# Optimization experiments

Hardware: AMD Instinct MI355X
Metric: run time of the kernel (lower is better)

The kernel has to match this reference:

```python
import jax, jax.numpy as jnp
import numpy as np

DIM = 768
HEADS = 12
HEAD_DIM = DIM // HEADS
EPS = 1e-5

def setup_inputs() -> dict:
    key = jax.random.key(0)
    ks = jax.random.split(key, 12)
    s = 1.0 / np.sqrt(DIM)
    x = jax.random.normal(ks[0], (4, 2048, DIM), dtype=jnp.float32)
    Wq = jax.random.uniform(ks[1], (DIM, DIM), jnp.float32, -s, s)
    bq = jnp.zeros((DIM,), jnp.float32)
    Wk = jax.random.uniform(ks[2], (DIM, DIM), jnp.float32, -s, s)
    bk = jnp.zeros((DIM,), jnp.float32)
    Wv = jax.random.uniform(ks[3], (DIM, DIM), jnp.float32, -s, s)
    bv = jnp.zeros((DIM,), jnp.float32)
    W1 = jax.random.uniform(ks[4], (DIM, 2 * DIM), jnp.float32, -s, s)
    b1 = jnp.zeros((2 * DIM,), jnp.float32)
    s2 = 1.0 / np.sqrt(2 * DIM)
    W2 = jax.random.uniform(ks[5], (2 * DIM, DIM), jnp.float32, -s2, s2)
    b2 = jnp.zeros((DIM,), jnp.float32)
    gamma = jnp.ones((DIM,), jnp.float32)
    beta = jnp.zeros((DIM,), jnp.float32)
    return {"x": x, "Wq": Wq, "bq": bq, "Wk": Wk, "bk": bk, "Wv": Wv, "bv": bv,
            "W1": W1, "b1": b1, "W2": W2, "b2": b2, "gamma": gamma, "beta": beta}

def reference(x, Wq, bq, Wk, bk, Wv, bv, W1, b1, W2, b2, gamma, beta):
    B, S, _ = x.shape
    # QKV projections -> (B, H, S, Dh)
    q = (x @ Wq + bq).reshape(B, S, HEADS, HEAD_DIM).transpose(0, 2, 1, 3)
    k = (x @ Wk + bk).reshape(B, S, HEADS, HEAD_DIM).transpose(0, 2, 1, 3)
    v = (x @ Wv + bv).reshape(B, S, HEADS, HEAD_DIM).transpose(0, 2, 1, 3)
    scores = jnp.einsum('bhqd,bhkd->bhqk', q, k) / jnp.sqrt(jnp.float32(HEAD_DIM))
    attn = jax.nn.softmax(scores, axis=-1)  # dropout is identity in eval
    ctx = jnp.einsum('bhqk,bhkd->bhqd', attn, v)
    ctx = ctx.transpose(0, 2, 1, 3).reshape(B, S, DIM)
    # MLP
    out = jax.nn.relu(ctx @ W1 + b1) @ W2 + b2
    # residual + LayerNorm
    h = x + out
    mu = jnp.mean(h, axis=-1, keepdims=True)
    var = jnp.mean(jnp.square(h - mu), axis=-1, keepdims=True)
    return (h - mu) * jax.lax.rsqrt(var + EPS) * gamma + beta
```

## Files before the change

### kernel.cpp

```cpp
#include <hip/hip_runtime.h>
#include <stdint.h>

#define DIM 768
#define HDIM 64
#define NHEADS 12
#define SEQ 2048
#define BATCH 4
#define NTOK (BATCH*SEQ)
#define FF 1536
#define QSCALE 0.1803368801111204f

typedef __bf16 bf16x8 __attribute__((ext_vector_type(8)));
typedef float f32x4 __attribute__((ext_vector_type(4)));
typedef unsigned short u16;
typedef unsigned int u32;

static __device__ __forceinline__ u16 f2bf(float f) {
  u32 u = __float_as_uint(f);
  u32 r = (u + 0x7fffu + ((u >> 16) & 1u)) >> 16;
  return (u16)r;
}

static __device__ __forceinline__ void async16(const void* g, void* l) {
  __builtin_amdgcn_global_load_lds(
      (const __attribute__((address_space(1))) u32*)g,
      (__attribute__((address_space(3))) u32*)l, 16, 0, 0);
}


__global__ void conv_bf16(const float* __restrict__ in, u16* __restrict__ out, int n) {
  int i = (blockIdx.x * 256 + threadIdx.x) * 4;
  if (i < n) {
    float4 f = *(const float4*)(in + i);
    uint2 o;
    o.x = (u32)f2bf(f.x) | ((u32)f2bf(f.y) << 16);
    o.y = (u32)f2bf(f.z) | ((u32)f2bf(f.w) << 16);
    *(uint2*)(out + i) = o;
  }
}

__global__ void prep_weights(const float* __restrict__ Wq, const float* __restrict__ Wk,
                             const float* __restrict__ Wv, const float* __restrict__ W1,
                             const float* __restrict__ W2, const float* __restrict__ bq,
                             const float* __restrict__ bk, const float* __restrict__ bv,
                             u16* __restrict__ Wqkvt, u16* __restrict__ W1t,
                             u16* __restrict__ W2t, float* __restrict__ bqkv) {
  const int bid = blockIdx.x;
  if (bid >= 4032) {
    int i = (bid - 4032) * 256 + threadIdx.x;
    if (i < DIM) bqkv[i] = bq[i];
    else if (i < 2 * DIM) bqkv[i] = bk[i - DIM];
    else if (i < 3 * DIM) bqkv[i] = bv[i - 2 * DIM];
    return;
  }
  const float* W; u16* dst; int K, N, tile;
  if (bid < 1728) {
    int z = bid / 576, t2 = bid - z * 576;
    W = z == 0 ? Wq : (z == 1 ? Wk : Wv);
    dst = Wqkvt + (size_t)z * DIM * DIM; K = DIM; N = DIM; tile = t2;
  } else if (bid < 2880) {
    W = W1; dst = W1t; K = DIM; N = FF; tile = bid - 1728;
  } else {
    W = W2; dst = W2t; K = FF; N = DIM; tile = bid - 2880;
  }
  const int ntx = N / 32;
  const int k0 = (tile / ntx) * 32, n0 = (tile - (tile / ntx) * ntx) * 32;
  __shared__ float t32[32][33];
  const int tx = threadIdx.x & 31, ty = threadIdx.x >> 5;
#pragma unroll
  for (int i = 0; i < 4; i++)
    t32[ty + 8 * i][tx] = W[(size_t)(k0 + ty + 8 * i) * N + n0 + tx];
  __syncthreads();
#pragma unroll
  for (int i = 0; i < 4; i++)
    dst[(size_t)(n0 + ty + 8 * i) * K + k0 + tx] = f2bf(t32[tx][ty + 8 * i]);
}


template<int MODE, int NT>
__launch_bounds__(256, 3)
__global__ void gemm128(const u16* __restrict__ A, const u16* __restrict__ Bt,
                        const float* __restrict__ bias, void* __restrict__ outp,
                        int K) {
  __shared__ u16 sA[128 * 64];
  __shared__ u16 sB[128 * 64];
  const int t = threadIdx.x;
  const int w = t >> 6;
  const int lane = t & 63;
  const int quad = lane >> 4;
  const int l15 = lane & 15;

  const int fid = blockIdx.x;
  const int xcd = fid & 7;
  const int j = fid >> 3;
  const int m0 = (xcd + 8 * (j / NT)) * 128;
  const int n0 = (j % NT) * 128;

  const int wr = (w & 1) * 64;
  const int wc = (w >> 1) * 64;

  f32x4 acc[4][4];
#pragma unroll
  for (int i = 0; i < 4; i++)
#pragma unroll
    for (int jj = 0; jj < 4; jj++) acc[i][jj] = (f32x4){0.f, 0.f, 0.f, 0.f};

  const int rowA = lane >> 3;
  const int colSw = ((lane & 7) ^ rowA) * 8;

  for (int k0 = 0; k0 < K; k0 += 64) {
    __syncthreads();
#pragma unroll
    for (int jj = 0; jj < 4; jj++) {
      int r0 = (jj * 4 + w) * 8;
      async16(A + (size_t)(m0 + r0 + rowA) * K + k0 + colSw, sA + r0 * 64);
      async16(Bt + (size_t)(n0 + r0 + rowA) * K + k0 + colSw, sB + r0 * 64);
    }
    __builtin_amdgcn_s_waitcnt(0);
    __syncthreads();
#pragma unroll
    for (int ks = 0; ks < 64; ks += 32) {
      bf16x8 a[4], b[4];
#pragma unroll
      for (int i = 0; i < 4; i++)
        a[i] = *(const bf16x8*)(sA + (wr + i * 16 + l15) * 64 +
                                ((((ks >> 3) + quad) ^ (l15 & 7)) * 8));
#pragma unroll
      for (int jj = 0; jj < 4; jj++)
        b[jj] = *(const bf16x8*)(sB + (wc + jj * 16 + l15) * 64 +
                                 ((((ks >> 3) + quad) ^ (l15 & 7)) * 8));
#pragma unroll
      for (int i = 0; i < 4; i++)
#pragma unroll
        for (int jj = 0; jj < 4; jj++)
          acc[i][jj] = __builtin_amdgcn_mfma_f32_16x16x32_bf16(a[i], b[jj], acc[i][jj], 0, 0, 0);
    }
  }

#pragma unroll
  for (int i = 0; i < 4; i++) {
#pragma unroll
    for (int jj = 0; jj < 4; jj++) {
#pragma unroll
      for (int r = 0; r < 4; r++) {
        int m = m0 + wr + i * 16 + quad * 4 + r;
        int n = n0 + wc + jj * 16 + l15;
        float v = acc[i][jj][r] + bias[n];
        if (MODE == 5) {
          int b = m >> 11, s = m & 2047;
          u16* o = (u16*)outp;
          if (n < DIM) {
            int h = n >> 6, d = n & 63;
            o[(((size_t)(b * NHEADS + h) * SEQ + s) << 6) + d] = f2bf(v * QSCALE);
          } else if (n < 2 * DIM) {
            int nn = n - DIM, h = nn >> 6, d = nn & 63;
            o[(size_t)NTOK * DIM + (((size_t)(b * NHEADS + h) * SEQ + s) << 6) + d] = f2bf(v);
          } else {
            int nn = n - 2 * DIM, h = nn >> 6, d = nn & 63;
            o[2 * (size_t)NTOK * DIM + ((size_t)(b * NHEADS + h) * HDIM + d) * SEQ + s] = f2bf(v);
          }
        } else if (MODE == 3) {
          ((u16*)outp)[(size_t)m * FF + n] = f2bf(fmaxf(v, 0.f));
        } else {
          ((float*)outp)[(size_t)m * DIM + n] = v;
        }
      }
    }
  }
}


__launch_bounds__(256, 3)
__global__ void attn(const u16* __restrict__ Q, const u16* __restrict__ Kb,
                     const u16* __restrict__ Vt, u16* __restrict__ Ctx) {
  __shared__ u16 sK[2][64 * 64];
  __shared__ u16 sV[2][64 * 64];
  __shared__ u16 sP[4][32 * 64];
  const int t = threadIdx.x, w = t >> 6, lane = t & 63;
  const int quad = lane >> 4, l15 = lane & 15;

  const int fid = blockIdx.x;
  const int xcd = fid & 7;
  const int idx = fid >> 3;
  const int bh = xcd + 8 * (idx >> 4);
  const int qb = idx & 15;
  const size_t qkbase = (size_t)bh * SEQ * HDIM;
  const int q0 = qb * 128 + w * 32;

  bf16x8 qf[2][2];
#pragma unroll
  for (int i = 0; i < 2; i++)
#pragma unroll
    for (int ks = 0; ks < 2; ks++)
      qf[i][ks] = *(const bf16x8*)(Q + qkbase + (size_t)(q0 + i * 16 + l15) * HDIM +
                                   ks * 32 + quad * 8);

  f32x4 o[2][4];
#pragma unroll
  for (int i = 0; i < 2; i++)
#pragma unroll
    for (int di = 0; di < 4; di++) o[i][di] = (f32x4){0.f, 0.f, 0.f, 0.f};
  float rs[2] = {0.f, 0.f};

  const int rowK = lane >> 3;
  const int colKsw = ((lane & 7) ^ rowK) * 8;
  const int swz = l15 & 7;

#define STAGE(kt, b) do {                                                          \
    int rr0 = w * 8, rr1 = (4 + w) * 8;                                            \
    async16(Kb + qkbase + (size_t)((kt) * 64 + rr0 + rowK) * HDIM + colKsw,        \
            sK[b] + rr0 * 64);                                                     \
    async16(Vt + qkbase + (size_t)(rr0 + rowK) * SEQ + (kt) * 64 + colKsw,         \
            sV[b] + rr0 * 64);                                                     \
    async16(Kb + qkbase + (size_t)((kt) * 64 + rr1 + rowK) * HDIM + colKsw,        \
            sK[b] + rr1 * 64);                                                     \
    async16(Vt + qkbase + (size_t)(rr1 + rowK) * SEQ + (kt) * 64 + colKsw,         \
            sV[b] + rr1 * 64);                                                     \
  } while (0)

  auto compute = [&](int cur) {
    const u16* kb = sK[cur];
    const u16* vb = sV[cur];
    u16* pw = sP[w];

    f32x4 sc[2][4];
    __builtin_amdgcn_s_setprio(1);
#pragma unroll
    for (int n4 = 0; n4 < 4; n4++) {
      int kr = n4 * 16;
      bf16x8 a0 = *(const bf16x8*)(kb + (kr + l15) * 64 + ((quad ^ swz) * 8));
      bf16x8 a1 = *(const bf16x8*)(kb + (kr + l15) * 64 + (((4 + quad) ^ swz) * 8));
#pragma unroll
      for (int i = 0; i < 2; i++) {
        f32x4 c = (f32x4){0.f, 0.f, 0.f, 0.f};
        c = __builtin_amdgcn_mfma_f32_16x16x32_bf16(a0, qf[i][0], c, 0, 0, 0);
        c = __builtin_amdgcn_mfma_f32_16x16x32_bf16(a1, qf[i][1], c, 0, 0, 0);
        sc[i][n4] = c;
      }
    }
    __builtin_amdgcn_s_setprio(0);

#pragma unroll
    for (int i = 0; i < 2; i++) {
      int row = i * 16 + l15;
#pragma unroll
      for (int n4 = 0; n4 < 4; n4++) {
        float p0 = __builtin_amdgcn_exp2f(sc[i][n4][0]);
        float p1 = __builtin_amdgcn_exp2f(sc[i][n4][1]);
        float p2 = __builtin_amdgcn_exp2f(sc[i][n4][2]);
        float p3 = __builtin_amdgcn_exp2f(sc[i][n4][3]);
        rs[i] += (p0 + p1) + (p2 + p3);
        u32 lo, hi;
        asm("v_cvt_pk_bf16_f32 %0, %1, %2" : "=v"(lo) : "v"(p0), "v"(p1));
        asm("v_cvt_pk_bf16_f32 %0, %1, %2" : "=v"(hi) : "v"(p2), "v"(p3));
        int cp = (n4 * 2 + (quad >> 1)) ^ swz;
        *(uint2*)(pw + row * 64 + cp * 8 + (quad & 1) * 4) = (uint2){lo, hi};
      }
    }

    __builtin_amdgcn_s_setprio(1);
#pragma unroll
    for (int ks = 0; ks < 2; ks++) {
      bf16x8 ap[2];
#pragma unroll
      for (int i = 0; i < 2; i++)
        ap[i] = *(const bf16x8*)(pw + (i * 16 + l15) * 64 + (((ks * 4 + quad) ^ swz) * 8));
#pragma unroll
      for (int di = 0; di < 4; di++) {
        bf16x8 b = *(const bf16x8*)(vb + (di * 16 + l15) * 64 +
                                    (((ks * 4 + quad) ^ swz) * 8));
        o[0][di] = __builtin_amdgcn_mfma_f32_16x16x32_bf16(ap[0], b, o[0][di], 0, 0, 0);
        o[1][di] = __builtin_amdgcn_mfma_f32_16x16x32_bf16(ap[1], b, o[1][di], 0, 0, 0);
      }
    }
    __builtin_amdgcn_s_setprio(0);
  };

  STAGE(0, 0);
  int cur = 0;
  for (int kt = 0; kt < SEQ / 64 - 1; kt++) {
    STAGE(kt + 1, cur ^ 1);
    asm volatile("s_waitcnt vmcnt(4)" ::: "memory");
    __builtin_amdgcn_s_barrier();
    compute(cur);
    __builtin_amdgcn_s_barrier();
    cur ^= 1;
  }
  asm volatile("s_waitcnt vmcnt(0)" ::: "memory");
  __builtin_amdgcn_s_barrier();
  compute(cur);
#undef STAGE

  float rsum[2];
#pragma unroll
  for (int i = 0; i < 2; i++) {
    float s = rs[i];
    s += __shfl_xor(s, 16);
    s += __shfl_xor(s, 32);
    rsum[i] = s;
  }
  int b = bh / NHEADS, h = bh - b * NHEADS;
#pragma unroll
  for (int i = 0; i < 2; i++) {
#pragma unroll
    for (int r = 0; r < 4; r++) {
      float inv = 1.f / __shfl(rsum[i], quad * 4 + r);
      int q = q0 + i * 16 + quad * 4 + r;
      size_t base = (size_t)(b * SEQ + q) * DIM + h * HDIM;
#pragma unroll
      for (int di = 0; di < 4; di++)
        Ctx[base + di * 16 + l15] = f2bf(o[i][di][r] * inv);
    }
  }
}


__launch_bounds__(256)
__global__ void ln_kernel(const float* __restrict__ x, const float* __restrict__ y,
                          const float* __restrict__ gamma, const float* __restrict__ beta,
                          float* __restrict__ out) {
  const int tok = blockIdx.x * 4 + (threadIdx.x >> 6);
  const int lane = threadIdx.x & 63;
  const float4* X = (const float4*)(x + (size_t)tok * DIM);
  const float4* Y = (const float4*)(y + (size_t)tok * DIM);
  const float4* G = (const float4*)gamma;
  const float4* Bt = (const float4*)beta;
  float4* O = (float4*)(out + (size_t)tok * DIM);

  float4 h[3];
  float s = 0.f;
#pragma unroll
  for (int i = 0; i < 3; i++) {
    float4 a = X[i * 64 + lane], b = Y[i * 64 + lane];
    h[i].x = a.x + b.x; h[i].y = a.y + b.y; h[i].z = a.z + b.z; h[i].w = a.w + b.w;
    s += h[i].x + h[i].y + h[i].z + h[i].w;
  }
#pragma unroll
  for (int off = 32; off >= 1; off >>= 1) s += __shfl_xor(s, off);
  float mu = s * (1.f / DIM);
  float v = 0.f;
#pragma unroll
  for (int i = 0; i < 3; i++) {
    h[i].x -= mu; h[i].y -= mu; h[i].z -= mu; h[i].w -= mu;
    v += h[i].x * h[i].x + h[i].y * h[i].y + h[i].z * h[i].z + h[i].w * h[i].w;
  }
#pragma unroll
  for (int off = 32; off >= 1; off >>= 1) v += __shfl_xor(v, off);
  float rstd = rsqrtf(v * (1.f / DIM) + 1e-5f);
#pragma unroll
  for (int i = 0; i < 3; i++) {
    float4 g = G[i * 64 + lane], bt = Bt[i * 64 + lane];
    float4 r;
    r.x = h[i].x * rstd * g.x + bt.x;
    r.y = h[i].y * rstd * g.y + bt.y;
    r.z = h[i].z * rstd * g.z + bt.z;
    r.w = h[i].w * rstd * g.w + bt.w;
    O[i * 64 + lane] = r;
  }
}


extern "C" void kernel_launch(void* const* d_in, const int* in_sizes, int n_in,
                              void* d_out, int out_size, void* d_ws, size_t ws_size,
                              hipStream_t stream) {
  const float* x  = (const float*)d_in[0];
  const float* Wq = (const float*)d_in[1];
  const float* bq = (const float*)d_in[2];
  const float* Wk = (const float*)d_in[3];
  const float* bk = (const float*)d_in[4];
  const float* Wv = (const float*)d_in[5];
  const float* bv = (const float*)d_in[6];
  const float* W1 = (const float*)d_in[7];
  const float* b1 = (const float*)d_in[8];
  const float* W2 = (const float*)d_in[9];
  const float* b2 = (const float*)d_in[10];
  const float* gamma = (const float*)d_in[11];
  const float* beta  = (const float*)d_in[12];

  char* ws = (char*)d_ws;
  u16* xb   = (u16*)ws;           ws += (size_t)NTOK * DIM * 2;
  u16* Wqkvt = (u16*)ws;          ws += (size_t)DIM * DIM * 3 * 2;
  u16* W1t  = (u16*)ws;           ws += (size_t)DIM * FF * 2;
  u16* W2t  = (u16*)ws;           ws += (size_t)DIM * FF * 2;
  float* bqkv = (float*)ws;       ws += (size_t)3 * DIM * 4;
  u16* Qb   = (u16*)ws;           ws += (size_t)NTOK * DIM * 2;
  u16* Kbf  = (u16*)ws;           ws += (size_t)NTOK * DIM * 2;
  u16* Vtb  = (u16*)ws;           ws += (size_t)NTOK * DIM * 2;
  u16* Ctx  = (u16*)ws;           ws += (size_t)NTOK * DIM * 2;
  u16* H1   = (u16*)ws;           ws += (size_t)NTOK * FF * 2;
  float* Y2 = (float*)ws;         ws += (size_t)NTOK * DIM * 4;

  conv_bf16<<<(NTOK * DIM) / 1024, 256, 0, stream>>>(x, xb, NTOK * DIM);
  prep_weights<<<4041, 256, 0, stream>>>(Wq, Wk, Wv, W1, W2, bq, bk, bv,
                                         Wqkvt, W1t, W2t, bqkv);

  gemm128<5, 18><<<1152, 256, 0, stream>>>(xb, Wqkvt, bqkv, Qb, DIM);

  attn<<<768, 256, 0, stream>>>(Qb, Kbf, Vtb, Ctx);

  gemm128<3, 12><<<768, 256, 0, stream>>>(Ctx, W1t, b1, H1, DIM);
  gemm128<4, 6><<<384, 256, 0, stream>>>(H1, W2t, b2, Y2, FF);

  ln_kernel<<<NTOK / 4, 256, 0, stream>>>(x, Y2, gamma, beta, (float*)d_out);
}
```

Measured before the change: 285.5 us.

## Double-buffer GEMM LDS tiles with async prefetch of next K slice

Splits the 128x64 LDS tiles into two 128x32 buffers and prefetches the next K slice with global_load_lds while the MFMAs run on the current one, waiting with a partial vmcnt instead of a full drain. It also raises wave priority around the MFMA block and uses a new XOR swizzle for the narrower rows. The aim is to hide global-memory latency behind compute, at the cost of twice as many barriers per unit of K and a smaller K step per iteration.

Measured after the change: 306.0 us. 7.2% more time.

```diff
diff --git a/kernel.cpp b/kernel.cpp
--- a/kernel.cpp
+++ b/kernel.cpp
@@ -82,8 +82,8 @@
 __global__ void gemm128(const u16* __restrict__ A, const u16* __restrict__ Bt,
                         const float* __restrict__ bias, void* __restrict__ outp,
                         int K) {
-  __shared__ u16 sA[128 * 64];
-  __shared__ u16 sB[128 * 64];
+  __shared__ u16 sA[2][128 * 32];
+  __shared__ u16 sB[2][128 * 32];
   const int t = threadIdx.x;
   const int w = t >> 6;
   const int lane = t & 63;
@@ -105,37 +105,54 @@
 #pragma unroll
     for (int jj = 0; jj < 4; jj++) acc[i][jj] = (f32x4){0.f, 0.f, 0.f, 0.f};
 
-  const int rowA = lane >> 3;
-  const int colSw = ((lane & 7) ^ rowA) * 8;
-
-  for (int k0 = 0; k0 < K; k0 += 64) {
-    __syncthreads();
-#pragma unroll
-    for (int jj = 0; jj < 4; jj++) {
-      int r0 = (jj * 4 + w) * 8;
-      async16(A + (size_t)(m0 + r0 + rowA) * K + k0 + colSw, sA + r0 * 64);
-      async16(Bt + (size_t)(n0 + r0 + rowA) * K + k0 + colSw, sB + r0 * 64);
-    }
-    __builtin_amdgcn_s_waitcnt(0);
-    __syncthreads();
-#pragma unroll
-    for (int ks = 0; ks < 64; ks += 32) {
-      bf16x8 a[4], b[4];
-#pragma unroll
-      for (int i = 0; i < 4; i++)
-        a[i] = *(const bf16x8*)(sA + (wr + i * 16 + l15) * 64 +
-                                ((((ks >> 3) + quad) ^ (l15 & 7)) * 8));
+  const int lrow = lane >> 2;
+  const int lchunk = (lane & 3) ^ ((lane >> 3) & 3);
+  const int R0 = w * 32;
+  const int fsw = (l15 >> 1) & 3;
+
+#define GSTAGE(k0v, b) do {                                                        \
+    async16(A + (size_t)(m0 + R0 + lrow) * K + (k0v) + lchunk * 8,                 \
+            sA[b] + R0 * 32);                                                      \
+    async16(Bt + (size_t)(n0 + R0 + lrow) * K + (k0v) + lchunk * 8,                \
+            sB[b] + R0 * 32);                                                      \
+    async16(A + (size_t)(m0 + R0 + 16 + lrow) * K + (k0v) + lchunk * 8,            \
+            sA[b] + (R0 + 16) * 32);                                               \
+    async16(Bt + (size_t)(n0 + R0 + 16 + lrow) * K + (k0v) + lchunk * 8,           \
+            sB[b] + (R0 + 16) * 32);                                               \
+  } while (0)
+
+  auto compute = [&](int cur) {
+    bf16x8 a[4], b[4];
+#pragma unroll
+    for (int i = 0; i < 4; i++)
+      a[i] = *(const bf16x8*)(sA[cur] + (wr + i * 16 + l15) * 32 + ((quad ^ fsw) * 8));
+#pragma unroll
+    for (int jj = 0; jj < 4; jj++)
+      b[jj] = *(const bf16x8*)(sB[cur] + (wc + jj * 16 + l15) * 32 + ((quad ^ fsw) * 8));
+    __builtin_amdgcn_s_setprio(1);
+#pragma unroll
+    for (int i = 0; i < 4; i++)
 #pragma unroll
       for (int jj = 0; jj < 4; jj++)
-        b[jj] = *(const bf16x8*)(sB + (wc + jj * 16 + l15) * 64 +
-                                 ((((ks >> 3) + quad) ^ (l15 & 7)) * 8));
-#pragma unroll
-      for (int i = 0; i < 4; i++)
-#pragma unroll
-        for (int jj = 0; jj < 4; jj++)
-          acc[i][jj] = __builtin_amdgcn_mfma_f32_16x16x32_bf16(a[i], b[jj], acc[i][jj], 0, 0, 0);
-    }
-  }
+        acc[i][jj] = __builtin_amdgcn_mfma_f32_16x16x32_bf16(a[i], b[jj], acc[i][jj], 0, 0, 0);
+    __builtin_amdgcn_s_setprio(0);
+  };
+
+  GSTAGE(0, 0);
+  int cur = 0;
+  const int iters = K >> 5;
+  for (int kt = 0; kt < iters - 1; kt++) {
+    GSTAGE((kt + 1) * 32, cur ^ 1);
+    asm volatile("s_waitcnt vmcnt(4)" ::: "memory");
+    __builtin_amdgcn_s_barrier();
+    compute(cur);
+    __builtin_amdgcn_s_barrier();
+    cur ^= 1;
+  }
+  asm volatile("s_waitcnt vmcnt(0)" ::: "memory");
+  __builtin_amdgcn_s_barrier();
+  compute(cur);
+#undef GSTAGE
 
 #pragma unroll
   for (int i = 0; i < 4; i++) {
```

## Split-K the W2 GEMM and widen QKV GEMM tile to eight waves

Applied to the files above, without the earlier changes.

The second MLP GEMM is split into two K halves, doubling its block count. Partial results are written to two fp32 buffers and summed inside the LayerNorm kernel, with the bias applied to only one half. The QKV projection now uses 512-thread blocks with a 128x256 tile, halving the block count and improving reuse of A. The cost is extra fp32 traffic for the second partial buffer and higher per-block resource use.

New measurement: 518.4 us. 81.6% more time.

```diff
diff --git a/kernel.cpp b/kernel.cpp
--- a/kernel.cpp
+++ b/kernel.cpp
@@ -77,13 +77,14 @@
 }
 
 
-template<int MODE, int NT>
-__launch_bounds__(256, 3)
+template<int MODE, int NT, int NW>
+__launch_bounds__(NW * 64, NW == 8 ? 6 : 3)
 __global__ void gemm128(const u16* __restrict__ A, const u16* __restrict__ Bt,
                         const float* __restrict__ bias, void* __restrict__ outp,
-                        int K) {
+                        int K, int ldk) {
+  constexpr int BN = 64 * (NW / 2);
   __shared__ u16 sA[128 * 64];
-  __shared__ u16 sB[128 * 64];
+  __shared__ u16 sB[BN * 64];
   const int t = threadIdx.x;
   const int w = t >> 6;
   const int lane = t & 63;
@@ -92,9 +93,12 @@
 
   const int fid = blockIdx.x;
   const int xcd = fid & 7;
-  const int j = fid >> 3;
+  int j = fid >> 3;
+  int kb = 0;
+  if (MODE == 6) { kb = j >= NT * 8; j -= kb * NT * 8; }
   const int m0 = (xcd + 8 * (j / NT)) * 128;
-  const int n0 = (j % NT) * 128;
+  const int n0 = (j % NT) * BN;
+  if (MODE == 6) { A += (size_t)kb * 768; Bt += (size_t)kb * 768; }
 
   const int wr = (w & 1) * 64;
   const int wc = (w >> 1) * 64;
@@ -111,10 +115,14 @@
   for (int k0 = 0; k0 < K; k0 += 64) {
     __syncthreads();
 #pragma unroll
-    for (int jj = 0; jj < 4; jj++) {
-      int r0 = (jj * 4 + w) * 8;
-      async16(A + (size_t)(m0 + r0 + rowA) * K + k0 + colSw, sA + r0 * 64);
-      async16(Bt + (size_t)(n0 + r0 + rowA) * K + k0 + colSw, sB + r0 * 64);
+    for (int s = 0; s < 128 / (8 * NW); s++) {
+      int r0 = (s * NW + w) * 8;
+      async16(A + (size_t)(m0 + r0 + rowA) * ldk + k0 + colSw, sA + r0 * 64);
+    }
+#pragma unroll
+    for (int s = 0; s < BN / (8 * NW); s++) {
+      int r0 = (s * NW + w) * 8;
+      async16(Bt + (size_t)(n0 + r0 + rowA) * ldk + k0 + colSw, sB + r0 * 64);
     }
     __builtin_amdgcn_s_waitcnt(0);
     __syncthreads();
@@ -145,8 +153,8 @@
       for (int r = 0; r < 4; r++) {
         int m = m0 + wr + i * 16 + quad * 4 + r;
         int n = n0 + wc + jj * 16 + l15;
-        float v = acc[i][jj][r] + bias[n];
         if (MODE == 5) {
+          float v = acc[i][jj][r] + bias[n];
           int b = m >> 11, s = m & 2047;
           u16* o = (u16*)outp;
           if (n < DIM) {
@@ -160,9 +168,12 @@
             o[2 * (size_t)NTOK * DIM + ((size_t)(b * NHEADS + h) * HDIM + d) * SEQ + s] = f2bf(v);
           }
         } else if (MODE == 3) {
-          ((u16*)outp)[(size_t)m * FF + n] = f2bf(fmaxf(v, 0.f));
+          ((u16*)outp)[(size_t)m * FF + n] = f2bf(fmaxf(acc[i][jj][r] + bias[n], 0.f));
+        } else if (MODE == 6) {
+          ((float*)outp)[(size_t)kb * NTOK * DIM + (size_t)m * DIM + n] =
+              acc[i][jj][r] + (kb ? 0.f : bias[n]);
         } else {
-          ((float*)outp)[(size_t)m * DIM + n] = v;
+          ((float*)outp)[(size_t)m * DIM + n] = acc[i][jj][r] + bias[n];
         }
       }
     }
@@ -316,13 +327,15 @@
 
 
 __launch_bounds__(256)
-__global__ void ln_kernel(const float* __restrict__ x, const float* __restrict__ y,
+__global__ void ln_kernel(const float* __restrict__ x, const float* __restrict__ ya,
+                          const float* __restrict__ yb,
                           const float* __restrict__ gamma, const float* __restrict__ beta,
                           float* __restrict__ out) {
   const int tok = blockIdx.x * 4 + (threadIdx.x >> 6);
   const int lane = threadIdx.x & 63;
   const float4* X = (const float4*)(x + (size_t)tok * DIM);
-  const float4* Y = (const float4*)(y + (size_t)tok * DIM);
+  const float4* Ya = (const float4*)(ya + (size_t)tok * DIM);
+  const float4* Yb = (const float4*)(yb + (size_t)tok * DIM);
   const float4* G = (const float4*)gamma;
   const float4* Bt = (const float4*)beta;
   float4* O = (float4*)(out + (size_t)tok * DIM);
@@ -331,8 +344,9 @@
   float s = 0.f;
 #pragma unroll
   for (int i = 0; i < 3; i++) {
-    float4 a = X[i * 64 + lane], b = Y[i * 64 + lane];
-    h[i].x = a.x + b.x; h[i].y = a.y + b.y; h[i].z = a.z + b.z; h[i].w = a.w + b.w;
+    float4 a = X[i * 64 + lane], b = Ya[i * 64 + lane], c = Yb[i * 64 + lane];
+    h[i].x = a.x + b.x + c.x; h[i].y = a.y + b.y + c.y;
+    h[i].z = a.z + b.z + c.z; h[i].w = a.w + b.w + c.w;
     s += h[i].x + h[i].y + h[i].z + h[i].w;
   }
 #pragma unroll
@@ -388,18 +402,19 @@
   u16* Vtb  = (u16*)ws;           ws += (size_t)NTOK * DIM * 2;
   u16* Ctx  = (u16*)ws;           ws += (size_t)NTOK * DIM * 2;
   u16* H1   = (u16*)ws;           ws += (size_t)NTOK * FF * 2;
-  float* Y2 = (float*)ws;         ws += (size_t)NTOK * DIM * 4;
+  float* Y2 = (float*)ws;         ws += (size_t)2 * NTOK * DIM * 4;
 
   conv_bf16<<<(NTOK * DIM) / 1024, 256, 0, stream>>>(x, xb, NTOK * DIM);
   prep_weights<<<4041, 256, 0, stream>>>(Wq, Wk, Wv, W1, W2, bq, bk, bv,
                                          Wqkvt, W1t, W2t, bqkv);
 
-  gemm128<5, 18><<<1152, 256, 0, stream>>>(xb, Wqkvt, bqkv, Qb, DIM);
+  gemm128<5, 9, 8><<<576, 512, 0, stream>>>(xb, Wqkvt, bqkv, Qb, DIM, DIM);
 
   attn<<<768, 256, 0, stream>>>(Qb, Kbf, Vtb, Ctx);
 
-  gemm128<3, 12><<<768, 256, 0, stream>>>(Ctx, W1t, b1, H1, DIM);
-  gemm128<4, 6><<<384, 256, 0, stream>>>(H1, W2t, b2, Y2, FF);
-
-  ln_kernel<<<NTOK / 4, 256, 0, stream>>>(x, Y2, gamma, beta, (float*)d_out);
-}
+  gemm128<3, 12, 4><<<768, 256, 0, stream>>>(Ctx, W1t, b1, H1, DIM, DIM);
+  gemm128<6, 6, 4><<<768, 256, 0, stream>>>(H1, W2t, b2, Y2, 768, FF);
+
+  ln_kernel<<<NTOK / 4, 256, 0, stream>>>(x, Y2, Y2 + (size_t)NTOK * DIM,
+                                          gamma, beta, (float*)d_out);
+}
```
